# Optimization experiments

Hardware: AMD Instinct MI355X
Metric: run time of the kernel (lower is better)

The kernel has to match this reference:

```python
import jax, jax.numpy as jnp
import numpy as np

B, K, W, H = 32, 64, 100, 150
ALPHA = 0.2        # leaky-relu slope
THRES = 2e-4       # causal threshold


def setup_inputs() -> dict:
    ks = jax.random.split(jax.random.key(0), 20)
    s = 0.1
    inp = {
        "x": jax.random.normal(ks[0], (B, K, W), jnp.float32),
        "y": jax.random.normal(ks[1], (B, K, 1), jnp.float32),
        "z_noise": jax.random.normal(ks[2], (B, H), jnp.float32),
        "lin_w": jax.random.normal(ks[3], (W, W), jnp.float32) * s,
        "lin_b": jax.random.normal(ks[4], (W,), jnp.float32) * s,
        "a": jax.random.normal(ks[5], (2, 1), jnp.float32),
        "bias": jax.random.normal(ks[6], (K, K * W), jnp.float32) * 0.01,
        "gl_wih": jax.random.normal(ks[7], (3 * H, W), jnp.float32) * s,
        "gl_whh": jax.random.normal(ks[8], (3 * H, H), jnp.float32) * s,
        "gl_bih": jax.random.normal(ks[9], (3 * H,), jnp.float32) * s,
        "gl_bhh": jax.random.normal(ks[10], (3 * H,), jnp.float32) * s,
        "mu_w": jax.random.normal(ks[11], (H, H), jnp.float32) * s,
        "mu_b": jax.random.normal(ks[12], (H,), jnp.float32) * s,
        "std_w": jax.random.normal(ks[13], (H, H), jnp.float32) * s,
        "std_b": jax.random.normal(ks[14], (H,), jnp.float32) * s,
        "net_wih": jax.random.normal(ks[15], (K, 3 * H, W), jnp.float32) * s,
        "net_whh": jax.random.normal(ks[16], (K, 3 * H, H), jnp.float32) * s,
        "net_bih": jax.random.normal(ks[17], (K, 3 * H), jnp.float32) * s,
        "net_bhh": jax.random.normal(ks[18], (K, 3 * H), jnp.float32) * s,
    }
    return inp


def _gru_last(wih, whh, bih, bhh, xs, h0):
    # xs: [B, S, in], h0: [B, H] -> final hidden [B, H]. PyTorch gate order r,z,n.
    gx = jnp.einsum('bsi,gi->sbg', xs, wih) + bih  # [S, B, 3H]
    h_dim = h0.shape[-1]

    def step(h, g):
        gh = h @ whh.T + bhh
        r = jax.nn.sigmoid(g[:, :h_dim] + gh[:, :h_dim])
        z = jax.nn.sigmoid(g[:, h_dim:2 * h_dim] + gh[:, h_dim:2 * h_dim])
        n = jnp.tanh(g[:, 2 * h_dim:] + r * gh[:, 2 * h_dim:])
        return (1.0 - z) * n + z * h, None

    h_last, _ = jax.lax.scan(step, h0, gx)
    return h_last


def reference(x, y, z_noise, lin_w, lin_b, a, bias, gl_wih, gl_whh, gl_bih, gl_bhh,
              mu_w, mu_b, std_w, std_b, net_wih, net_whh, net_bih, net_bhh):
    xw = x[:, :, -W:]
    Wx = xw @ lin_w.T + lin_b                       # [B, K, W]
    v = Wx.reshape(Wx.shape[0], K * W)              # [B, K*W]
    # e = a_input @ a, where a_input[...,0]=y broadcast, a_input[...,1]=v tiled per node
    e = a[0, 0] * y + a[1, 0] * v[:, None, :] + bias  # [B, K, K*W]
    e = jax.nn.leaky_relu(e, ALPHA)
    attention = jax.nn.softmax(e, axis=2)           # dropout p=0 -> identity
    A = attention >= THRES                           # [B, K, K*W] mask
    Ax = jnp.where(A, v[:, None, :], 0.0)
    cause_x = Wx + Ax.sum(axis=2, keepdims=True)    # [B, K, W]
    # left GRU over the node dimension (seq len = K)
    h0 = jnp.zeros((cause_x.shape[0], H), cause_x.dtype)
    h_t = _gru_last(gl_wih, gl_whh, gl_bih, gl_bhh, cause_x, h0)  # [B, H]
    mu = h_t @ mu_w.T + mu_b
    log_var = h_t @ std_w.T + std_b
    sigma = jnp.exp(0.5 * log_var)
    z = mu + sigma * z_noise                        # [B, H]
    # K independent GRUs, same input Wx and same init state z -> vmap over weights
    causes = jax.vmap(lambda wi, wh, bi, bh: _gru_last(wi, wh, bi, bh, Wx, z))(
        net_wih, net_whh, net_bih, net_bhh)         # [K, B, H]
    return causes.transpose(1, 0, 2)                # [B, K, H]
```

## Files before the change

kernel.cpp:

```cpp
#include <hip/hip_runtime.h>

#define Bc 32
#define Kc 64
#define Wc 100
#define Hc 150
#define H3c 450
#define KWc 6400
#define ALPHAc 0.2f
#define THRESc 0.0002f

typedef unsigned int u32;
typedef unsigned short u16;
typedef __attribute__((ext_vector_type(8))) short short8;
typedef __attribute__((ext_vector_type(4))) float floatx4;

#define OFF_WX      0u
#define OFF_CS      204800u
#define OFF_GX      206848u
#define OFF_HT      1128448u
#define OFF_Z       1133248u

__device__ __forceinline__ float us2f(u16 u){ u32 x=((u32)u)<<16; return __uint_as_float(x); }
__device__ __forceinline__ u16 f2us(float f){
  u32 x = __float_as_uint(f);
  u32 r = (x + 0x7fffu + ((x>>16)&1u)) >> 16;
  return (u16)r;
}

__device__ __forceinline__ void lds_barrier(){
  __builtin_amdgcn_sched_barrier(0);
  asm volatile("s_waitcnt lgkmcnt(0)" ::: "memory");
  __builtin_amdgcn_s_barrier();
  __builtin_amdgcn_sched_barrier(0);
}

__global__ void wx_kernel(const float* __restrict__ x, const float* __restrict__ lin_w,
                          const float* __restrict__ lin_b, float* __restrict__ ws){
  int o = blockIdx.x*256 + threadIdx.x;
  if (o >= Bc*KWc) return;
  int i = o % Wc;
  int bk = o / Wc;
  const float4* xr = (const float4*)(x + bk*Wc);
  const float4* wr = (const float4*)(lin_w + i*Wc);
  float acc = lin_b[i];
  #pragma unroll
  for (int j=0;j<25;j++){
    float4 xv = xr[j], wv = wr[j];
    acc += xv.x*wv.x + xv.y*wv.y + xv.z*wv.z + xv.w*wv.w;
  }
  ws[OFF_WX + o] = acc;
}

__global__ void attn_kernel(const float* __restrict__ y, const float* __restrict__ a,
                            const float* __restrict__ bias, float* __restrict__ ws){
  __shared__ __align__(16) float e_l[KWc];
  __shared__ float red[4];
  int row = blockIdx.x;
  int b = row >> 6, k = row & 63;
  int tid = threadIdx.x;
  float a0 = a[0], a1 = a[1];
  float yv = y[row];
  const float4* v4  = (const float4*)(ws + OFF_WX + (size_t)b*KWc);
  const float4* br4 = (const float4*)(bias + (size_t)k*KWc);
  float4* e4 = (float4*)e_l;
  float ay = a0*yv;
  float m = -3.4e38f;
  for (int j=tid; j<KWc/4; j+=256){
    float4 vv = v4[j], bb = br4[j];
    float4 e;
    e.x = ay + a1*vv.x + bb.x; e.x = (e.x>=0.f)?e.x:ALPHAc*e.x;
    e.y = ay + a1*vv.y + bb.y; e.y = (e.y>=0.f)?e.y:ALPHAc*e.y;
    e.z = ay + a1*vv.z + bb.z; e.z = (e.z>=0.f)?e.z:ALPHAc*e.z;
    e.w = ay + a1*vv.w + bb.w; e.w = (e.w>=0.f)?e.w:ALPHAc*e.w;
    e4[j] = e;
    m = fmaxf(m, fmaxf(fmaxf(e.x,e.y), fmaxf(e.z,e.w)));
  }
  for (int o=32;o;o>>=1) m = fmaxf(m, __shfl_down(m, o));
  if ((tid&63)==0) red[tid>>6] = m;
  __syncthreads();
  m = fmaxf(fmaxf(red[0],red[1]), fmaxf(red[2],red[3]));
  __syncthreads();
  float ssum = 0.f;
  for (int j=tid; j<KWc/4; j+=256){
    float4 e = e4[j];
    ssum += __expf(e.x-m) + __expf(e.y-m) + __expf(e.z-m) + __expf(e.w-m);
  }
  for (int o=32;o;o>>=1) ssum += __shfl_down(ssum, o);
  if ((tid&63)==0) red[tid>>6] = ssum;
  __syncthreads();
  float s = red[0]+red[1]+red[2]+red[3];
  float thr = m + logf(THRESc * s);
  float cs = 0.f;
  for (int j=tid; j<KWc/4; j+=256){
    float4 e = e4[j];
    float4 vv = v4[j];
    if (e.x >= thr) cs += vv.x;
    if (e.y >= thr) cs += vv.y;
    if (e.z >= thr) cs += vv.z;
    if (e.w >= thr) cs += vv.w;
  }
  for (int o=32;o;o>>=1) cs += __shfl_down(cs, o);
  if ((tid&63)==0) red[tid>>6] = cs;
  __syncthreads();
  if (tid==0) ws[OFF_CS + row] = red[0]+red[1]+red[2]+red[3];
}

__global__ void glproj_kernel(const float* __restrict__ gl_wih, const float* __restrict__ gl_bih,
                              float* __restrict__ ws){
  int o = blockIdx.x*256 + threadIdx.x;
  if (o >= Kc*Bc*H3c) return;
  int g = o % H3c;
  int t = o / H3c;
  int b = t & 31, s = t >> 5;
  float cs = ws[OFF_CS + b*Kc + s];
  const float4* xr = (const float4*)(ws + OFF_WX + b*KWc + s*Wc);
  const float4* wr = (const float4*)(gl_wih + g*Wc);
  float acc = gl_bih[g];
  #pragma unroll
  for (int j=0;j<25;j++){
    float4 wv = wr[j], xv = xr[j];
    acc += (xv.x+cs)*wv.x + (xv.y+cs)*wv.y + (xv.z+cs)*wv.z + (xv.w+cs)*wv.w;
  }
  ws[OFF_GX + o] = acc;
}

__global__ void __launch_bounds__(512,1) glgru4_kernel(
    const float* __restrict__ gl_whh, const float* __restrict__ gl_bhh,
    float* __restrict__ ws){
  __shared__ __align__(16) u16 bF[10*16*40];
  __shared__ float g_l[480*10];
  int b0 = blockIdx.x*8;
  int tid = threadIdx.x;
  int w = tid >> 6, lane = tid & 63, quad = lane >> 4, n16 = lane & 15;

  short8 whhA[4][5];
  #pragma unroll
  for (int ti=0; ti<4; ti++){
    int tile = w*4 + ti;
    int sec = tile/10;
    int sr = (tile - sec*10)*16 + n16;
    bool rowok = (tile < 30) && (sr < Hc);
    int grow = sec*Hc + sr;
    const float* wr = gl_whh + (size_t)grow*Hc;
    #pragma unroll
    for (int c=0;c<5;c++){
      union { short8 v; u16 u[8]; } t8;
      #pragma unroll
      for (int j2=0;j2<4;j2++){
        int kk2 = c*32 + quad*8 + j2*2;
        float2 wv = (rowok && (kk2+1) < Hc) ? *(const float2*)(wr + kk2) : make_float2(0.f,0.f);
        t8.u[j2*2]   = f2us(wv.x);
        t8.u[j2*2+1] = f2us(wv.y);
      }
      whhA[ti][c] = t8.v;
    }
  }
  for (int i=tid; i<10*16*40/2; i+=512) ((u32*)bF)[i] = 0u;

  float hst[3] = {0.f,0.f,0.f};
  float bh_r[3], bh_z[3], bh_n[3];
  int tT[3], tBL[3];
  #pragma unroll
  for (int q=0;q<3;q++){
    int task = tid + q*512;
    if (task < 1200){
      int bl = task/150, t = task - bl*150;
      tT[q] = t; tBL[q] = bl;
      bh_r[q] = gl_bhh[t];
      bh_z[q] = gl_bhh[Hc+t];
      bh_n[q] = gl_bhh[2*Hc+t];
    } else { tT[q] = 0; tBL[q] = -1; }
  }

  for (int s=0;s<Kc;s++){
    lds_barrier();
    float gxr[3], gxz[3], gxn[3];
    const float* gxb = ws + OFF_GX + (size_t)(s*Bc)*H3c;
    #pragma unroll
    for (int q=0;q<3;q++){
      if (tBL[q] >= 0){
        const float* gp = gxb + (size_t)(b0+tBL[q])*H3c;
        int t = tT[q];
        gxr[q] = gp[t]; gxz[q] = gp[Hc+t]; gxn[q] = gp[2*Hc+t];
      }
    }
    const u16* bBase = bF + (size_t)n16*40 + (size_t)quad*8;
    short8 bh[10];
    #pragma unroll
    for (int c=0;c<10;c++) bh[c] = *(const short8*)(bBase + (size_t)c*640);
    floatx4 acc[4] = {{0.f,0.f,0.f,0.f},{0.f,0.f,0.f,0.f},{0.f,0.f,0.f,0.f},{0.f,0.f,0.f,0.f}};
    #pragma unroll
    for (int c=0;c<10;c++){
      int ca = (c<5)? c : (c-5);
      #pragma unroll
      for (int ti=0;ti<4;ti++)
        acc[ti] = __builtin_amdgcn_mfma_f32_16x16x32_bf16(whhA[ti][ca], bh[c], acc[ti], 0,0,0);
    }
    if (n16 < 8){
      #pragma unroll
      for (int ti=0;ti<4;ti++){
        int tile = w*4 + ti;
        if (tile < 30){
          int row0 = tile*16 + quad*4;
          float* gp = g_l + row0*10 + n16;
          #pragma unroll
          for (int r=0;r<4;r++) gp[r*10] = acc[ti][r];
        }
      }
    }
    lds_barrier();
    float grv[3], gzv[3], gnv[3];
    #pragma unroll
    for (int q=0;q<3;q++){
      if (tBL[q] >= 0){
        int t = tT[q], bl = tBL[q];
        grv[q] = g_l[t*10+bl];
        gzv[q] = g_l[(160+t)*10+bl];
        gnv[q] = g_l[(320+t)*10+bl];
      }
    }
    #pragma unroll
    for (int q=0;q<3;q++){
      if (tBL[q] >= 0){
        int t = tT[q], bl = tBL[q];
        float a_r = gxr[q] + grv[q] + bh_r[q];
        float a_z = gxz[q] + gzv[q] + bh_z[q];
        float r  = 1.f/(1.f+__expf(-a_r));
        float zz = 1.f/(1.f+__expf(-a_z));
        float nx = gxn[q] + r*(gnv[q] + bh_n[q]);
        nx = fminf(fmaxf(nx,-15.f),15.f);
        float e2 = __expf(2.f*nx);
        float n = (e2-1.f)/(e2+1.f);
        float h = (1.f-zz)*n + zz*hst[q];
        hst[q] = h;
        u16 hi = f2us(h); float hif = us2f(hi); u16 lo = f2us(h - hif);
        bF[(t>>5)*640 + bl*40 + (t&31)] = hi;
        bF[(5+(t>>5))*640 + bl*40 + (t&31)] = lo;
      }
    }
  }
  #pragma unroll
  for (int q=0;q<3;q++){
    if (tBL[q] >= 0)
      ws[OFF_HT + (size_t)(b0+tBL[q])*Hc + tT[q]] = hst[q];
  }
}

__global__ void z_kernel(const float* __restrict__ z_noise, const float* __restrict__ mu_w,
                         const float* __restrict__ mu_b, const float* __restrict__ std_w,
                         const float* __restrict__ std_b, float* __restrict__ ws){
  int o = blockIdx.x*256 + threadIdx.x;
  if (o >= Bc*Hc) return;
  int t = o % Hc, b = o / Hc;
  const float* h = ws + OFF_HT + b*Hc;
  const float2* mwr = (const float2*)(mu_w + t*Hc);
  const float2* swr = (const float2*)(std_w + t*Hc);
  float mu = mu_b[t], lv = std_b[t];
  for (int j=0;j<Hc/2;j++){
    float2 mw = mwr[j], sw = swr[j];
    float h0 = h[2*j], h1 = h[2*j+1];
    mu += h0*mw.x + h1*mw.y;
    lv += h0*sw.x + h1*sw.y;
  }
  float sg = expf(0.5f*lv);
  ws[OFF_Z + o] = mu + sg*z_noise[o];
}

__global__ void __launch_bounds__(512,1) causes3_kernel(
    const float* __restrict__ net_wih, const float* __restrict__ net_whh,
    const float* __restrict__ net_bih, const float* __restrict__ net_bhh,
    const float* __restrict__ ws, float* __restrict__ out){
  __shared__ __align__(16) u16 bF[14*16*40];
  __shared__ float g_rz[320*10];
  __shared__ float g_nh[160*10];
  __shared__ float g_np[160*10];
  int kk = blockIdx.x & 63, bg = blockIdx.x >> 6, b0 = bg*8;
  int tid = threadIdx.x;
  int w = tid >> 6, lane = tid & 63, quad = lane >> 4, n16 = lane & 15;
  const float* whhk = net_whh + (size_t)kk*H3c*Hc;
  const float* wihk = net_wih + (size_t)kk*H3c*Wc;
  const float* bihk = net_bih + kk*H3c;
  const float* bhhk = net_bhh + kk*H3c;

  short8 whhA[4][5], wihA[4][4];
  #pragma unroll
  for (int ti=0; ti<4; ti++){
    int tile = w*4 + ti;
    int sec = tile/10;
    int sr = (tile - sec*10)*16 + n16;
    bool rowok = (tile < 30) && (sr < Hc);
    int grow = sec*Hc + sr;
    #pragma unroll
    for (int c=0;c<5;c++){
      union { short8 v; u16 u[8]; } t8;
      #pragma unroll
      for (int j=0;j<8;j++){
        int k = c*32 + quad*8 + j;
        float v = (rowok && k < Hc) ? whhk[(size_t)grow*Hc + k] : 0.f;
        t8.u[j] = f2us(v);
      }
      whhA[ti][c] = t8.v;
    }
    #pragma unroll
    for (int c=0;c<4;c++){
      union { short8 v; u16 u[8]; } t8;
      #pragma unroll
      for (int j=0;j<8;j++){
        int k = c*32 + quad*8 + j;
        float v = (rowok && k < Wc) ? wihk[(size_t)grow*Wc + k] : 0.f;
        t8.u[j] = f2us(v);
      }
      wihA[ti][c] = t8.v;
    }
  }

  for (int i=tid; i<14*16*40/2; i+=512) ((u32*)bF)[i] = 0u;

  float hst[3] = {0.f,0.f,0.f};
  float brz_r[3], brz_z[3], bnh_[3], bnp_[3];
  #pragma unroll
  for (int q=0;q<3;q++){
    int task = tid + q*512;
    if (task < 1200){
      int t = task >> 3, bb = task & 7;
      float h = ws[OFF_Z + (b0+bb)*Hc + t];
      hst[q] = h;
      brz_r[q] = bhhk[t]      + bihk[t];
      brz_z[q] = bhhk[Hc+t]   + bihk[Hc+t];
      bnh_[q]  = bhhk[2*Hc+t];
      bnp_[q]  = bihk[2*Hc+t];
      u16 hi = f2us(h); float hif = us2f(hi); u16 lo = f2us(h - hif);
      bF[(t>>5)*640 + bb*40 + (t&31)] = hi;
      bF[(5+(t>>5))*640 + bb*40 + (t&31)] = lo;
    }
  }
  for (int it=tid; it<800; it+=512){
    int bb = it/100, i = it - bb*100;
    float xv = ws[OFF_WX + (b0+bb)*KWc + i];
    bF[(10+(i>>5))*640 + bb*40 + (i&31)] = f2us(xv);
  }

  int bb0 = tid/100, i0 = tid - bb0*100;
  int it1 = tid + 512;
  int bb1 = it1/100, i1 = it1 - bb1*100;
  bool v1ok = (it1 < 800);

  const bool isN = (w >= 5);
  for (int s=0;s<Kc;s++){
    float xp0 = 0.f, xp1 = 0.f;
    if (s < Kc-1){
      xp0 = ws[OFF_WX + (size_t)(b0+bb0)*KWc + (s+1)*Wc + i0];
      if (v1ok) xp1 = ws[OFF_WX + (size_t)(b0+bb1)*KWc + (s+1)*Wc + i1];
    }
    lds_barrier();
    const u16* bBase = bF + (size_t)n16*40 + (size_t)quad*8;
    short8 bx[4];
    #pragma unroll
    for (int c=0;c<4;c++) bx[c] = *(const short8*)(bBase + (size_t)(10+c)*640);
    floatx4 acc[4] = {{0.f,0.f,0.f,0.f},{0.f,0.f,0.f,0.f},{0.f,0.f,0.f,0.f},{0.f,0.f,0.f,0.f}};
    #pragma unroll
    for (int ca=0;ca<4;ca++){
      #pragma unroll
      for (int ti=0;ti<4;ti++)
        acc[ti] = __builtin_amdgcn_mfma_f32_16x16x32_bf16(wihA[ti][ca], bx[ca], acc[ti], 0,0,0);
    }
    __builtin_amdgcn_sched_barrier(0);
    short8 bh0[5];
    #pragma unroll
    for (int c=0;c<5;c++) bh0[c] = *(const short8*)(bBase + (size_t)c*640);
    if (isN){
      if (n16 < 8){
        #pragma unroll
        for (int ti=0;ti<4;ti++){
          int tile = w*4 + ti;
          if (tile < 30){
            int srb = (tile - 20)*16 + quad*4;
            float* gq = g_np + srb*10 + n16;
            #pragma unroll
            for (int r=0;r<4;r++) gq[r*10] = acc[ti][r];
          }
        }
      }
      #pragma unroll
      for (int ti=0;ti<4;ti++) acc[ti] = (floatx4){0.f,0.f,0.f,0.f};
    }
    #pragma unroll
    for (int c=0;c<5;c++){
      #pragma unroll
      for (int ti=0;ti<4;ti++)
        acc[ti] = __builtin_amdgcn_mfma_f32_16x16x32_bf16(whhA[ti][c], bh0[c], acc[ti], 0,0,0);
    }
    __builtin_amdgcn_sched_barrier(0);
    short8 bh1[5];
    #pragma unroll
    for (int c=0;c<5;c++) bh1[c] = *(const short8*)(bBase + (size_t)(5+c)*640);
    #pragma unroll
    for (int c=0;c<5;c++){
      #pragma unroll
      for (int ti=0;ti<4;ti++)
        acc[ti] = __builtin_amdgcn_mfma_f32_16x16x32_bf16(whhA[ti][c], bh1[c], acc[ti], 0,0,0);
    }
    if (n16 < 8){
      #pragma unroll
      for (int ti=0;ti<4;ti++){
        int tile = w*4 + ti;
        if (tile < 30){
          int sec = tile/10;
          int srb = (tile - sec*10)*16 + quad*4;
          if (sec < 2){
            float* gp = g_rz + (sec*160 + srb)*10 + n16;
            #pragma unroll
            for (int r=0;r<4;r++) gp[r*10] = acc[ti][r];
          } else {
            float* gh = g_nh + srb*10 + n16;
            #pragma unroll
            for (int r=0;r<4;r++) gh[r*10] = acc[ti][r];
          }
        }
      }
    }
    lds_barrier();
    #pragma unroll
    for (int q=0;q<3;q++){
      int task = tid + q*512;
      if (task < 1200){
        int t = task >> 3, bb = task & 7;
        float a_r = g_rz[t*10+bb] + brz_r[q];
        float a_z = g_rz[(160+t)*10+bb] + brz_z[q];
        float r  = 1.f/(1.f+__expf(-a_r));
        float zz = 1.f/(1.f+__expf(-a_z));
        float nx = (g_np[t*10+bb] + bnp_[q]) + r*(g_nh[t*10+bb] + bnh_[q]);
        nx = fminf(fmaxf(nx,-15.f),15.f);
        float e2 = __expf(2.f*nx);
        float n = (e2-1.f)/(e2+1.f);
        float h = (1.f-zz)*n + zz*hst[q];
        hst[q] = h;
        u16 hi = f2us(h); float hif = us2f(hi); u16 lo = f2us(h - hif);
        bF[(t>>5)*640 + bb*40 + (t&31)] = hi;
        bF[(5+(t>>5))*640 + bb*40 + (t&31)] = lo;
      }
    }
    if (s < Kc-1){
      bF[(10+(i0>>5))*640 + bb0*40 + (i0&31)] = f2us(xp0);
      if (v1ok) bF[(10+(i1>>5))*640 + bb1*40 + (i1&31)] = f2us(xp1);
    }
  }
  #pragma unroll
  for (int q=0;q<3;q++){
    int task = tid + q*512;
    if (task < 1200){
      int t = task >> 3, bb = task & 7;
      out[((size_t)(b0+bb)*Kc + kk)*Hc + t] = hst[q];
    }
  }
}

extern "C" void kernel_launch(void* const* d_in, const int* in_sizes, int n_in,
                              void* d_out, int out_size, void* d_ws, size_t ws_size,
                              hipStream_t stream){
  const float* x        = (const float*)d_in[0];
  const float* y        = (const float*)d_in[1];
  const float* z_noise  = (const float*)d_in[2];
  const float* lin_w    = (const float*)d_in[3];
  const float* lin_b    = (const float*)d_in[4];
  const float* a        = (const float*)d_in[5];
  const float* bias     = (const float*)d_in[6];
  const float* gl_wih   = (const float*)d_in[7];
  const float* gl_whh   = (const float*)d_in[8];
  const float* gl_bih   = (const float*)d_in[9];
  const float* gl_bhh   = (const float*)d_in[10];
  const float* mu_w     = (const float*)d_in[11];
  const float* mu_b     = (const float*)d_in[12];
  const float* std_w    = (const float*)d_in[13];
  const float* std_b    = (const float*)d_in[14];
  const float* net_wih  = (const float*)d_in[15];
  const float* net_whh  = (const float*)d_in[16];
  const float* net_bih  = (const float*)d_in[17];
  const float* net_bhh  = (const float*)d_in[18];
  float* ws = (float*)d_ws;
  float* out = (float*)d_out;

  wx_kernel<<<(Bc*KWc+255)/256, 256, 0, stream>>>(x, lin_w, lin_b, ws);
  attn_kernel<<<Bc*Kc, 256, 0, stream>>>(y, a, bias, ws);
  glproj_kernel<<<(Kc*Bc*H3c+255)/256, 256, 0, stream>>>(gl_wih, gl_bih, ws);
  glgru4_kernel<<<4, 512, 0, stream>>>(gl_whh, gl_bhh, ws);
  z_kernel<<<(Bc*Hc+255)/256, 256, 0, stream>>>(z_noise, mu_w, mu_b, std_w, std_b, ws);
  causes3_kernel<<<Kc*4, 512, 0, stream>>>(net_wih, net_whh, net_bih, net_bhh, ws, out);
}
```

Before: 493.6 us.

## Pack bf16 hi/lo hidden-state halves into unused MFMA B columns

The hidden state was split into bf16 hi and lo parts stored in separate LDS chunks, which needed two passes of MFMAs over the recurrent weights. Now the lo part goes into columns 8-15 of the same 16-wide B tile, which were previously unused padding since only 8 batch columns exist. A single MFMA pass plus a cross-lane shuffle-add (xor 8) merges hi and lo. This halves the recurrent MFMA count and B-operand LDS reads in both GRU kernels, at the cost of shuffles and some changed scheduling (sched barriers removed).

```diff
diff --git a/kernel.cpp b/kernel.cpp
--- a/kernel.cpp
+++ b/kernel.cpp
@@ -127,7 +127,7 @@
 __global__ void __launch_bounds__(512,1) glgru4_kernel(
     const float* __restrict__ gl_whh, const float* __restrict__ gl_bhh,
     float* __restrict__ ws){
-  __shared__ __align__(16) u16 bF[10*16*40];
+  __shared__ __align__(16) u16 bF[5*16*40];
   __shared__ float g_l[480*10];
   int b0 = blockIdx.x*8;
   int tid = threadIdx.x;
@@ -140,7 +140,7 @@
     int sec = tile/10;
     int sr = (tile - sec*10)*16 + n16;
     bool rowok = (tile < 30) && (sr < Hc);
-    int grow = sec*Hc + sr;
+    int grow = (sec<3 ? sec : 2)*Hc + sr;
     const float* wr = gl_whh + (size_t)grow*Hc;
     #pragma unroll
     for (int c=0;c<5;c++){
@@ -155,7 +155,7 @@
       whhA[ti][c] = t8.v;
     }
   }
-  for (int i=tid; i<10*16*40/2; i+=512) ((u32*)bF)[i] = 0u;
+  for (int i=tid; i<5*16*40/2; i+=512) ((u32*)bF)[i] = 0u;
 
   float hst[3] = {0.f,0.f,0.f};
   float bh_r[3], bh_z[3], bh_n[3];
@@ -185,16 +185,20 @@
       }
     }
     const u16* bBase = bF + (size_t)n16*40 + (size_t)quad*8;
-    short8 bh[10];
-    #pragma unroll
-    for (int c=0;c<10;c++) bh[c] = *(const short8*)(bBase + (size_t)c*640);
+    short8 bh[5];
+    #pragma unroll
+    for (int c=0;c<5;c++) bh[c] = *(const short8*)(bBase + (size_t)c*640);
     floatx4 acc[4] = {{0.f,0.f,0.f,0.f},{0.f,0.f,0.f,0.f},{0.f,0.f,0.f,0.f},{0.f,0.f,0.f,0.f}};
     #pragma unroll
-    for (int c=0;c<10;c++){
-      int ca = (c<5)? c : (c-5);
+    for (int c=0;c<5;c++){
       #pragma unroll
       for (int ti=0;ti<4;ti++)
-        acc[ti] = __builtin_amdgcn_mfma_f32_16x16x32_bf16(whhA[ti][ca], bh[c], acc[ti], 0,0,0);
+        acc[ti] = __builtin_amdgcn_mfma_f32_16x16x32_bf16(whhA[ti][c], bh[c], acc[ti], 0,0,0);
+    }
+    #pragma unroll
+    for (int ti=0;ti<4;ti++){
+      #pragma unroll
+      for (int r=0;r<4;r++) acc[ti][r] += __shfl_xor(acc[ti][r], 8);
     }
     if (n16 < 8){
       #pragma unroll
@@ -235,7 +239,7 @@
         hst[q] = h;
         u16 hi = f2us(h); float hif = us2f(hi); u16 lo = f2us(h - hif);
         bF[(t>>5)*640 + bl*40 + (t&31)] = hi;
-        bF[(5+(t>>5))*640 + bl*40 + (t&31)] = lo;
+        bF[(t>>5)*640 + (bl+8)*40 + (t&31)] = lo;
       }
     }
   }
@@ -270,7 +274,7 @@
     const float* __restrict__ net_wih, const float* __restrict__ net_whh,
     const float* __restrict__ net_bih, const float* __restrict__ net_bhh,
     const float* __restrict__ ws, float* __restrict__ out){
-  __shared__ __align__(16) u16 bF[14*16*40];
+  __shared__ __align__(16) u16 bF[9*16*40];
   __shared__ float g_rz[320*10];
   __shared__ float g_nh[160*10];
   __shared__ float g_np[160*10];
@@ -289,7 +293,7 @@
     int sec = tile/10;
     int sr = (tile - sec*10)*16 + n16;
     bool rowok = (tile < 30) && (sr < Hc);
-    int grow = sec*Hc + sr;
+    int grow = (sec<3 ? sec : 2)*Hc + sr;
     #pragma unroll
     for (int c=0;c<5;c++){
       union { short8 v; u16 u[8]; } t8;
@@ -314,7 +318,7 @@
     }
   }
 
-  for (int i=tid; i<14*16*40/2; i+=512) ((u32*)bF)[i] = 0u;
+  for (int i=tid; i<9*16*40/2; i+=512) ((u32*)bF)[i] = 0u;
 
   float hst[3] = {0.f,0.f,0.f};
   float brz_r[3], brz_z[3], bnh_[3], bnp_[3];
@@ -331,13 +335,13 @@
       bnp_[q]  = bihk[2*Hc+t];
       u16 hi = f2us(h); float hif = us2f(hi); u16 lo = f2us(h - hif);
       bF[(t>>5)*640 + bb*40 + (t&31)] = hi;
-      bF[(5+(t>>5))*640 + bb*40 + (t&31)] = lo;
+      bF[(t>>5)*640 + (bb+8)*40 + (t&31)] = lo;
     }
   }
   for (int it=tid; it<800; it+=512){
     int bb = it/100, i = it - bb*100;
     float xv = ws[OFF_WX + (b0+bb)*KWc + i];
-    bF[(10+(i>>5))*640 + bb*40 + (i&31)] = f2us(xv);
+    bF[(5+(i>>5))*640 + bb*40 + (i&31)] = f2us(xv);
   }
 
   int bb0 = tid/100, i0 = tid - bb0*100;
@@ -356,7 +360,10 @@
     const u16* bBase = bF + (size_t)n16*40 + (size_t)quad*8;
     short8 bx[4];
     #pragma unroll
-    for (int c=0;c<4;c++) bx[c] = *(const short8*)(bBase + (size_t)(10+c)*640);
+    for (int c=0;c<4;c++) bx[c] = *(const short8*)(bBase + (size_t)(5+c)*640);
+    short8 bh[5];
+    #pragma unroll
+    for (int c=0;c<5;c++) bh[c] = *(const short8*)(bBase + (size_t)c*640);
     floatx4 acc[4] = {{0.f,0.f,0.f,0.f},{0.f,0.f,0.f,0.f},{0.f,0.f,0.f,0.f},{0.f,0.f,0.f,0.f}};
     #pragma unroll
     for (int ca=0;ca<4;ca++){
@@ -364,10 +371,6 @@
       for (int ti=0;ti<4;ti++)
         acc[ti] = __builtin_amdgcn_mfma_f32_16x16x32_bf16(wihA[ti][ca], bx[ca], acc[ti], 0,0,0);
     }
-    __builtin_amdgcn_sched_barrier(0);
-    short8 bh0[5];
-    #pragma unroll
-    for (int c=0;c<5;c++) bh0[c] = *(const short8*)(bBase + (size_t)c*640);
     if (isN){
       if (n16 < 8){
         #pragma unroll
@@ -388,17 +391,12 @@
     for (int c=0;c<5;c++){
       #pragma unroll
       for (int ti=0;ti<4;ti++)
-        acc[ti] = __builtin_amdgcn_mfma_f32_16x16x32_bf16(whhA[ti][c], bh0[c], acc[ti], 0,0,0);
-    }
-    __builtin_amdgcn_sched_barrier(0);
-    short8 bh1[5];
-    #pragma unroll
-    for (int c=0;c<5;c++) bh1[c] = *(const short8*)(bBase + (size_t)(5+c)*640);
-    #pragma unroll
-    for (int c=0;c<5;c++){
-      #pragma unroll
-      for (int ti=0;ti<4;ti++)
-        acc[ti] = __builtin_amdgcn_mfma_f32_16x16x32_bf16(whhA[ti][c], bh1[c], acc[ti], 0,0,0);
+        acc[ti] = __builtin_amdgcn_mfma_f32_16x16x32_bf16(whhA[ti][c], bh[c], acc[ti], 0,0,0);
+    }
+    #pragma unroll
+    for (int ti=0;ti<4;ti++){
+      #pragma unroll
+      for (int r=0;r<4;r++) acc[ti][r] += __shfl_xor(acc[ti][r], 8);
     }
     if (n16 < 8){
       #pragma unroll
@@ -437,12 +435,12 @@
         hst[q] = h;
         u16 hi = f2us(h); float hif = us2f(hi); u16 lo = f2us(h - hif);
         bF[(t>>5)*640 + bb*40 + (t&31)] = hi;
-        bF[(5+(t>>5))*640 + bb*40 + (t&31)] = lo;
+        bF[(t>>5)*640 + (bb+8)*40 + (t&31)] = lo;
       }
     }
     if (s < Kc-1){
-      bF[(10+(i0>>5))*640 + bb0*40 + (i0&31)] = f2us(xp0);
-      if (v1ok) bF[(10+(i1>>5))*640 + bb1*40 + (i1&31)] = f2us(xp1);
+      bF[(5+(i0>>5))*640 + bb0*40 + (i0&31)] = f2us(xp0);
+      if (v1ok) bF[(5+(i1>>5))*640 + bb1*40 + (i1&31)] = f2us(xp1);
     }
   }
   #pragma unroll
```

Result: no change. 488.7 us (-1.0%).
